# Kernel tuning notes

Hardware: AMD Instinct MI355X
Metric: run time of the kernel (lower is better)

Reference implementation:

```python
import jax, jax.numpy as jnp
import numpy as np
from jax.ops import segment_sum, segment_max

B, L, D, H, DK, NL, V, FF = 8, 256, 256, 8, 32, 4, 2048, 1024
N = B * L
EPS = 1e-5


def _ln(x, g, b):
    m = jnp.mean(x, -1, keepdims=True)
    v = jnp.var(x, -1, keepdims=True)
    return (x - m) * jax.lax.rsqrt(v + EPS) * g + b


def setup_inputs() -> dict:
    key = jax.random.key(0)
    ks = list(jax.random.split(key, 16))
    # causal decoder-decoder edges, sorted by destination (DGL 'dd' eids)
    dst_seq = np.repeat(np.arange(L), np.arange(L) + 1)
    src_seq = np.concatenate([np.arange(j + 1) for j in range(L)])
    src = jnp.asarray(np.concatenate([src_seq + b * L for b in range(B)]), jnp.int32)
    dst = jnp.asarray(np.concatenate([dst_seq + b * L for b in range(B)]), jnp.int32)
    tokens = jax.random.randint(ks[0], (N,), 0, V)
    positions = jnp.tile(jnp.arange(L), B)  # tgt[1]
    s = 0.02
    nrm = lambda k, sh: jax.random.normal(k, sh, jnp.float32) * s
    return {
        'tokens': tokens, 'positions': positions, 'src': src, 'dst': dst,
        'value_tab': nrm(ks[1], (V, D)),
        'coord_tab': nrm(ks[2], (3, D)),
        'pos_tab': nrm(ks[3], (L, D)),
        'ln1_g': jnp.ones((NL, D), jnp.float32), 'ln1_b': jnp.zeros((NL, D), jnp.float32),
        'Wq': nrm(ks[4], (NL, D, D)), 'Wk': nrm(ks[5], (NL, D, D)),
        'Wv': nrm(ks[6], (NL, D, D)), 'Wo': nrm(ks[7], (NL, D, D)),
        'ln2_g': jnp.ones((NL, D), jnp.float32), 'ln2_b': jnp.zeros((NL, D), jnp.float32),
        'W1': nrm(ks[8], (NL, D, FF)), 'b1': jnp.zeros((NL, FF), jnp.float32),
        'W2': nrm(ks[9], (NL, FF, D)), 'b2': jnp.zeros((NL, D), jnp.float32),
        'lnf_g': jnp.ones((D,), jnp.float32), 'lnf_b': jnp.zeros((D,), jnp.float32),
        'Wgen': nrm(ks[10], (D, V)), 'bgen': jnp.zeros((V,), jnp.float32),
    }


def reference(tokens, positions, src, dst, value_tab, coord_tab, pos_tab,
              ln1_g, ln1_b, Wq, Wk, Wv, Wo, ln2_g, ln2_b,
              W1, b1, W2, b2, lnf_g, lnf_b, Wgen, bgen):
    # embeddings: value*sqrt(d) + coord(pos%3) + pos(pos//3)
    x = value_tab[tokens] * jnp.sqrt(jnp.float32(D)) \
        + coord_tab[positions % 3] + pos_tab[positions // 3]
    inv_sqrt_dk = 1.0 / jnp.sqrt(jnp.float32(DK))
    for i in range(NL):
        # pre_func: layernorm + qkv projection, split heads
        xn = _ln(x, ln1_g[i], ln1_b[i])
        q = (xn @ Wq[i]).reshape(N, H, DK)
        k = (xn @ Wk[i]).reshape(N, H, DK)
        v = (xn @ Wv[i]).reshape(N, H, DK)
        # apply_edges(u_dot_v): per-edge, per-head score
        score = jnp.einsum('ehd,ehd->eh', k[src], q[dst]) * inv_sqrt_dk  # [E,H]
        # edge_softmax over edges grouped by destination node
        m = jax.lax.stop_gradient(
            segment_max(score, dst, num_segments=N, indices_are_sorted=True))
        a = jnp.exp(score - m[dst])
        denom = segment_sum(a, dst, num_segments=N, indices_are_sorted=True)
        alpha = a / denom[dst]  # [E,H]
        # send_and_recv(u_mul_e -> sum): softmax-weighted aggregation
        z = segment_sum(v[src] * alpha[..., None], dst,
                        num_segments=N, indices_are_sorted=True).reshape(N, D)
        # post_func: output proj + residual, then FFN sublayer
        x = x + z @ Wo[i]
        xn2 = _ln(x, ln2_g[i], ln2_b[i])
        x = x + (jax.nn.relu(xn2 @ W1[i] + b1[i]) @ W2[i] + b2[i])
    x = _ln(x, lnf_g, lnf_b)
    return jax.nn.log_softmax(x @ Wgen + bgen, axis=-1)  # generator
```

## Files before the change

kernel.cpp:

```cpp
#include <hip/hip_runtime.h>
#include <hip/hip_bf16.h>
#include <math.h>

constexpr int B_ = 8, L_ = 256, D_ = 256, H_ = 8, DK_ = 32, NL_ = 4, V_ = 2048, FF_ = 1024;
constexpr int N_ = B_ * L_;
constexpr float EPS_ = 1e-5f;
constexpr int LDW_ = 56;

typedef short bf16x8 __attribute__((ext_vector_type(8)));
typedef float f32x4 __attribute__((ext_vector_type(4)));
typedef _Float16 f16x4 __attribute__((ext_vector_type(4)));

__device__ __forceinline__ short f2b(float f) {
    union { __hip_bfloat16 h; short s; } u;
    u.h = __float2bfloat16(f);
    return u.s;
}

__global__ void transpose_all(const float* __restrict__ Wq, const float* __restrict__ Wk,
                              const float* __restrict__ Wv, const float* __restrict__ Wo,
                              const float* __restrict__ W1, const float* __restrict__ W2,
                              const float* __restrict__ Wgen,
                              short* __restrict__ wqT, short* __restrict__ wkT,
                              short* __restrict__ wvT, short* __restrict__ woT,
                              short* __restrict__ w1T, short* __restrict__ w2T,
                              short* __restrict__ wgT,
                              const int* __restrict__ tokens, const int* __restrict__ positions,
                              const float* __restrict__ vtab, const float* __restrict__ ctab,
                              const float* __restrict__ ptab, float* __restrict__ x) {
    __shared__ float tile[32][33];
    int id = blockIdx.x;
    if (id >= 3584) {
        int n = id - 3584;
        int d = threadIdx.y * 32 + threadIdx.x;
        int tok = tokens[n], p = positions[n];
        x[n * D_ + d] = vtab[tok * D_ + d] * 16.0f + ctab[(p % 3) * D_ + d] + ptab[(p / 3) * D_ + d];
        return;
    }
    const float* src;
    short* dst;
    int K, Nn, tx, ty;
    if (id < 1024) {
        int m = id >> 8, rem = id & 255, layer = rem >> 6, tt = rem & 63;
        K = 256; Nn = 256; tx = tt & 7; ty = tt >> 3;
        size_t off = (size_t)layer * 256 * 256;
        if (m == 0) { src = Wq + off; dst = wqT + off; }
        else if (m == 1) { src = Wk + off; dst = wkT + off; }
        else if (m == 2) { src = Wv + off; dst = wvT + off; }
        else { src = Wo + off; dst = woT + off; }
    } else if (id < 2048) {
        int rem = id - 1024, layer = rem >> 8, tt = rem & 255;
        K = 256; Nn = 1024; tx = tt & 31; ty = tt >> 5;
        size_t off = (size_t)layer * 256 * 1024;
        src = W1 + off; dst = w1T + off;
    } else if (id < 3072) {
        int rem = id - 2048, layer = rem >> 8, tt = rem & 255;
        K = 1024; Nn = 256; tx = tt & 7; ty = tt >> 3;
        size_t off = (size_t)layer * 1024 * 256;
        src = W2 + off; dst = w2T + off;
    } else {
        int tt = id - 3072;
        K = 256; Nn = 2048; tx = tt & 63; ty = tt >> 6;
        src = Wgen; dst = wgT;
    }
    int n0 = tx * 32, k0 = ty * 32;
    int x_ = threadIdx.x, y_ = threadIdx.y;
#pragma unroll
    for (int i = 0; i < 32; i += 8)
        tile[y_ + i][x_] = src[(size_t)(k0 + y_ + i) * Nn + n0 + x_];
    __syncthreads();
#pragma unroll
    for (int i = 0; i < 32; i += 8)
        dst[(size_t)(n0 + y_ + i) * K + k0 + x_] = f2b(tile[x_][y_ + i]);
}

__device__ __forceinline__ int4 pack8(const float* v) {
    union { short s[8]; int4 q; } u;
#pragma unroll
    for (int j = 0; j < 8; ++j) u.s[j] = f2b(v[j]);
    return u.q;
}

template <int EPI, bool HAS_BIAS>
__device__ __forceinline__ void gemm_epilogue(f32x4 acc00, f32x4 acc01, f32x4 acc10, f32x4 acc11,
                                              const float* __restrict__ bias, float* __restrict__ Cf,
                                              short* __restrict__ Cb, int Nout, int kz,
                                              int m0, int n0, int mo, int no, int quad, int r) {
#pragma unroll
    for (int i = 0; i < 2; ++i) {
#pragma unroll
        for (int j = 0; j < 2; ++j) {
            f32x4 acc = (i == 0) ? (j == 0 ? acc00 : acc01) : (j == 0 ? acc10 : acc11);
            int col = n0 + no + j * 16 + r;
            float bval = HAS_BIAS ? bias[col] : 0.f;
#pragma unroll
            for (int p = 0; p < 4; ++p) {
                int row = m0 + mo + i * 16 + quad * 4 + p;
                float v = acc[p];
                if (EPI == 1) {
                    Cb[(size_t)row * Nout + col] = f2b(fmaxf(v + bval, 0.f));
                } else if (EPI == 2) {
                    float add = v + ((HAS_BIAS && kz == 0) ? bval : 0.f);
                    atomicAdd(&Cf[(size_t)row * Nout + col], add);
                } else if (EPI == 3) {
                    Cf[(size_t)row * Nout + col] = v + bval;
                } else if (EPI == 4) {
                    Cb[(size_t)row * Nout + col] = f2b(v);
                } else {
                    ((_Float16*)Cb)[(size_t)row * Nout + col] = (_Float16)v;
                }
            }
        }
    }
}

template <int EPI, bool HAS_BIAS>
__device__ __forceinline__ void gemm_body(const short* __restrict__ A, const short* __restrict__ Bt,
                                          const float* __restrict__ bias, float* __restrict__ Cf,
                                          short* __restrict__ Cb, int M, int K, int Nout,
                                          int kbeg, int kend, int kz) {
    __shared__ short As[2][64][LDW_];
    __shared__ short Bs[2][64][LDW_];
    int t = threadIdx.x;
    int m0 = blockIdx.x * 64, n0 = blockIdx.y * 64;
    int sr = t >> 2, sc = (t & 3) * 8;
    int lane = t & 63, w = t >> 6;
    int mo = (w & 1) * 32, no = (w >> 1) * 32;
    int quad = lane >> 4, r = lane & 15;
    f32x4 acc00 = {}, acc01 = {}, acc10 = {}, acc11 = {};
    const short* Ap = &A[(size_t)(m0 + sr) * K + sc];
    const short* Bp = &Bt[(size_t)(n0 + sr) * K + sc];
    int4 av = *(const int4*)(Ap + kbeg);
    int4 bv = *(const int4*)(Bp + kbeg);
    *(int4*)&As[0][sr][sc] = av;
    *(int4*)&Bs[0][sr][sc] = bv;
    if (kbeg + 32 < kend) {
        av = *(const int4*)(Ap + kbeg + 32);
        bv = *(const int4*)(Bp + kbeg + 32);
    }
    __syncthreads();
    int p = 0;
    for (int k0 = kbeg; k0 < kend; k0 += 32, p ^= 1) {
        if (k0 + 32 < kend) {
            *(int4*)&As[p ^ 1][sr][sc] = av;
            *(int4*)&Bs[p ^ 1][sr][sc] = bv;
            if (k0 + 64 < kend) {
                av = *(const int4*)(Ap + k0 + 64);
                bv = *(const int4*)(Bp + k0 + 64);
            }
        }
        bf16x8 a0 = *(const bf16x8*)&As[p][mo + r][quad * 8];
        bf16x8 a1 = *(const bf16x8*)&As[p][mo + 16 + r][quad * 8];
        bf16x8 b0 = *(const bf16x8*)&Bs[p][no + r][quad * 8];
        bf16x8 b1 = *(const bf16x8*)&Bs[p][no + 16 + r][quad * 8];
        acc00 = __builtin_amdgcn_mfma_f32_16x16x32_bf16(a0, b0, acc00, 0, 0, 0);
        acc01 = __builtin_amdgcn_mfma_f32_16x16x32_bf16(a0, b1, acc01, 0, 0, 0);
        acc10 = __builtin_amdgcn_mfma_f32_16x16x32_bf16(a1, b0, acc10, 0, 0, 0);
        acc11 = __builtin_amdgcn_mfma_f32_16x16x32_bf16(a1, b1, acc11, 0, 0, 0);
        if (k0 + 32 < kend) __syncthreads();
    }
    gemm_epilogue<EPI, HAS_BIAS>(acc00, acc01, acc10, acc11, bias, Cf, Cb, Nout, kz,
                                 m0, n0, mo, no, quad, r);
}

template <int EPI, bool HAS_BIAS>
__device__ __forceinline__ void gemm_ln_body(const float* __restrict__ X,
                                             const float* __restrict__ lg, const float* __restrict__ lb,
                                             const short* __restrict__ Bt,
                                             const float* __restrict__ bias, float* __restrict__ Cf,
                                             short* __restrict__ Cb, int Nout) {
    __shared__ short As[2][64][LDW_];
    __shared__ short Bs[2][64][LDW_];
    __shared__ float gs[256], bs_[256];
    int t = threadIdx.x;
    int m0 = blockIdx.x * 64, n0 = blockIdx.y * 64;
    int sr = t >> 2, sc = (t & 3) * 8;
    int lane = t & 63, w = t >> 6;
    int mo = (w & 1) * 32, no = (w >> 1) * 32;
    int quad = lane >> 4, r = lane & 15;

    float xv[64];
    const float* xp = &X[(size_t)(m0 + sr) * 256 + sc];
#pragma unroll
    for (int c = 0; c < 8; ++c) {
        *(float4*)&xv[c * 8] = *(const float4*)(xp + c * 32);
        *(float4*)&xv[c * 8 + 4] = *(const float4*)(xp + c * 32 + 4);
    }
    const short* Bp = &Bt[(size_t)(n0 + sr) * 256 + sc];
    int4 bv = *(const int4*)Bp;
    gs[t] = lg[t];
    bs_[t] = lb[t];

    float s1 = 0.f, s2 = 0.f;
#pragma unroll
    for (int j = 0; j < 64; ++j) {
        s1 += xv[j];
        s2 += xv[j] * xv[j];
    }
    s1 += __shfl_xor(s1, 1, 64); s1 += __shfl_xor(s1, 2, 64);
    s2 += __shfl_xor(s2, 1, 64); s2 += __shfl_xor(s2, 2, 64);
    float mean = s1 * (1.0f / 256.0f);
    float inv = rsqrtf(s2 * (1.0f / 256.0f) - mean * mean + EPS_);
    __syncthreads();

    int4 a_regs[8];
#pragma unroll
    for (int c = 0; c < 8; ++c) {
        float tmp[8];
#pragma unroll
        for (int j = 0; j < 8; ++j)
            tmp[j] = (xv[c * 8 + j] - mean) * inv * gs[c * 32 + sc + j] + bs_[c * 32 + sc + j];
        a_regs[c] = pack8(tmp);
    }

    *(int4*)&As[0][sr][sc] = a_regs[0];
    *(int4*)&Bs[0][sr][sc] = bv;
    bv = *(const int4*)(Bp + 32);
    __syncthreads();

    f32x4 acc00 = {}, acc01 = {}, acc10 = {}, acc11 = {};
#pragma unroll
    for (int c = 0; c < 8; ++c) {
        int p = c & 1;
        if (c + 1 < 8) {
            *(int4*)&As[p ^ 1][sr][sc] = a_regs[c + 1];
            *(int4*)&Bs[p ^ 1][sr][sc] = bv;
            if (c + 2 < 8) bv = *(const int4*)(Bp + (c + 2) * 32);
        }
        bf16x8 a0 = *(const bf16x8*)&As[p][mo + r][quad * 8];
        bf16x8 a1 = *(const bf16x8*)&As[p][mo + 16 + r][quad * 8];
        bf16x8 b0 = *(const bf16x8*)&Bs[p][no + r][quad * 8];
        bf16x8 b1 = *(const bf16x8*)&Bs[p][no + 16 + r][quad * 8];
        acc00 = __builtin_amdgcn_mfma_f32_16x16x32_bf16(a0, b0, acc00, 0, 0, 0);
        acc01 = __builtin_amdgcn_mfma_f32_16x16x32_bf16(a0, b1, acc01, 0, 0, 0);
        acc10 = __builtin_amdgcn_mfma_f32_16x16x32_bf16(a1, b0, acc10, 0, 0, 0);
        acc11 = __builtin_amdgcn_mfma_f32_16x16x32_bf16(a1, b1, acc11, 0, 0, 0);
        if (c + 1 < 8) __syncthreads();
    }
    gemm_epilogue<EPI, HAS_BIAS>(acc00, acc01, acc10, acc11, bias, Cf, Cb, Nout, 0,
                                 m0, n0, mo, no, quad, r);
}

__global__ __launch_bounds__(256) void gemm_ln_qkv(const float* __restrict__ X,
                                                   const float* __restrict__ lg, const float* __restrict__ lb,
                                                   const short* __restrict__ wq, const short* __restrict__ wk,
                                                   const short* __restrict__ wv,
                                                   short* __restrict__ q, short* __restrict__ k,
                                                   short* __restrict__ v) {
    if (blockIdx.z == 0)
        gemm_ln_body<4, false>(X, lg, lb, wq, nullptr, nullptr, q, D_);
    else if (blockIdx.z == 1)
        gemm_ln_body<4, false>(X, lg, lb, wk, nullptr, nullptr, k, D_);
    else
        gemm_ln_body<5, false>(X, lg, lb, wv, nullptr, nullptr, v, D_);
}

__global__ __launch_bounds__(256) void gemm_ln_relu(const float* __restrict__ X,
                                                    const float* __restrict__ lg, const float* __restrict__ lb,
                                                    const short* __restrict__ Bt, const float* __restrict__ bias,
                                                    short* __restrict__ C) {
    gemm_ln_body<1, true>(X, lg, lb, Bt, bias, nullptr, C, FF_);
}

__global__ __launch_bounds__(256) void gemm_ln_bias(const float* __restrict__ X,
                                                    const float* __restrict__ lg, const float* __restrict__ lb,
                                                    const short* __restrict__ Bt, const float* __restrict__ bias,
                                                    float* __restrict__ C) {
    gemm_ln_body<3, true>(X, lg, lb, Bt, bias, C, nullptr, V_);
}

template <int SPLITK, bool HAS_BIAS>
__global__ __launch_bounds__(256) void gemm_accum(const short* __restrict__ A, const short* __restrict__ Bt,
                                                  const float* __restrict__ bias, float* __restrict__ C,
                                                  int M, int K, int Nout) {
    int Kp = K / SPLITK;
    int kz = blockIdx.z;
    gemm_body<2, HAS_BIAS>(A, Bt, bias, C, nullptr, M, K, Nout, kz * Kp, kz * Kp + Kp, kz);
}

__global__ __launch_bounds__(64) void attn_kernel(const short* __restrict__ q,
                                                  const short* __restrict__ k,
                                                  const _Float16* __restrict__ v,
                                                  short* __restrict__ z) {
    int blk = blockIdx.x;
    int bh = blk & 63;
    int qt = 15 - (blk >> 6);
    int b = bh >> 3, h = bh & 7;
    int lane = threadIdx.x;
    int r = lane & 15, quad = lane >> 4;
    int row0 = b * L_;

    bf16x8 qf = *(const bf16x8*)&q[(size_t)(row0 + qt * 16 + r) * D_ + h * DK_ + quad * 8];
    f32x4 O0 = {}, O1 = {};
    float mA = -1e30f, den = 0.f;
    int nk = qt + 1;

    bf16x8 kf = *(const bf16x8*)&k[(size_t)(row0 + r) * D_ + h * DK_ + quad * 8];
    f16x4 va, vb;
    {
        const _Float16* vp = v + (size_t)(row0 + quad * 4) * D_ + h * DK_;
#pragma unroll
        for (int i = 0; i < 4; ++i) {
            va[i] = vp[(size_t)i * D_ + r];
            vb[i] = vp[(size_t)i * D_ + 16 + r];
        }
    }
    for (int kt = 0; kt < nk; ++kt) {
        bf16x8 kf_n = kf;
        f16x4 va_n = va, vb_n = vb;
        if (kt + 1 < nk) {
            kf_n = *(const bf16x8*)&k[(size_t)(row0 + (kt + 1) * 16 + r) * D_ + h * DK_ + quad * 8];
            const _Float16* vp = v + (size_t)(row0 + (kt + 1) * 16 + quad * 4) * D_ + h * DK_;
#pragma unroll
            for (int i = 0; i < 4; ++i) {
                va_n[i] = vp[(size_t)i * D_ + r];
                vb_n[i] = vp[(size_t)i * D_ + 16 + r];
            }
        }
        f32x4 zero = {};
        f32x4 s = __builtin_amdgcn_mfma_f32_16x16x32_bf16(kf, qf, zero, 0, 0, 0);
#pragma unroll
        for (int i2 = 0; i2 < 4; ++i2) s[i2] *= 0.17677669529663687f;
        if (kt == qt) {
#pragma unroll
            for (int i2 = 0; i2 < 4; ++i2)
                if (quad * 4 + i2 > r) s[i2] = -1e30f;
        }
        float tmax = fmaxf(fmaxf(s[0], s[1]), fmaxf(s[2], s[3]));
        tmax = fmaxf(tmax, __shfl_xor(tmax, 16, 64));
        tmax = fmaxf(tmax, __shfl_xor(tmax, 32, 64));
        float mn = fmaxf(mA, tmax);
        float alpha = __expf(mA - mn);
        mA = mn;
        float p0 = __expf(s[0] - mn), p1 = __expf(s[1] - mn);
        float p2 = __expf(s[2] - mn), p3 = __expf(s[3] - mn);
        float ts = (p0 + p1) + (p2 + p3);
        ts += __shfl_xor(ts, 16, 64);
        ts += __shfl_xor(ts, 32, 64);
        den = den * alpha + ts;
        f16x4 pf;
        pf[0] = (_Float16)p0; pf[1] = (_Float16)p1; pf[2] = (_Float16)p2; pf[3] = (_Float16)p3;
        float al[4];
#pragma unroll
        for (int i2 = 0; i2 < 4; ++i2) al[i2] = __shfl(alpha, quad * 4 + i2, 64);
#pragma unroll
        for (int i2 = 0; i2 < 4; ++i2) { O0[i2] *= al[i2]; O1[i2] *= al[i2]; }
        O0 = __builtin_amdgcn_mfma_f32_16x16x16f16(pf, va, O0, 0, 0, 0);
        O1 = __builtin_amdgcn_mfma_f32_16x16x16f16(pf, vb, O1, 0, 0, 0);
        kf = kf_n; va = va_n; vb = vb_n;
    }
#pragma unroll
    for (int i2 = 0; i2 < 4; ++i2) {
        float inv = 1.0f / __shfl(den, quad * 4 + i2, 64);
        int rowz = row0 + qt * 16 + quad * 4 + i2;
        z[(size_t)rowz * D_ + h * DK_ + r] = f2b(O0[i2] * inv);
        z[(size_t)rowz * D_ + h * DK_ + 16 + r] = f2b(O1[i2] * inv);
    }
}

__global__ void lsm_kernel(float* __restrict__ logits) {
    __shared__ float rm[4], rs[4];
    int row = blockIdx.x, t = threadIdx.x;
    float* p = logits + (size_t)row * V_;
    float vals[8];
    float mx = -INFINITY;
#pragma unroll
    for (int i = 0; i < 8; ++i) {
        vals[i] = p[t + i * 256];
        mx = fmaxf(mx, vals[i]);
    }
#pragma unroll
    for (int off = 32; off; off >>= 1) mx = fmaxf(mx, __shfl_xor(mx, off, 64));
    int w = t >> 6;
    if ((t & 63) == 0) rm[w] = mx;
    __syncthreads();
    mx = fmaxf(fmaxf(rm[0], rm[1]), fmaxf(rm[2], rm[3]));
    float s = 0.f;
#pragma unroll
    for (int i = 0; i < 8; ++i) s += __expf(vals[i] - mx);
#pragma unroll
    for (int off = 32; off; off >>= 1) s += __shfl_xor(s, off, 64);
    if ((t & 63) == 0) rs[w] = s;
    __syncthreads();
    s = rs[0] + rs[1] + rs[2] + rs[3];
    float lse = mx + logf(s);
#pragma unroll
    for (int i = 0; i < 8; ++i) p[t + i * 256] = vals[i] - lse;
}

extern "C" void kernel_launch(void* const* d_in, const int* in_sizes, int n_in,
                              void* d_out, int out_size, void* d_ws, size_t ws_size,
                              hipStream_t stream) {
    const int* tokens = (const int*)d_in[0];
    const int* positions = (const int*)d_in[1];
    const float* vtab = (const float*)d_in[4];
    const float* ctab = (const float*)d_in[5];
    const float* ptab = (const float*)d_in[6];
    const float* ln1_g = (const float*)d_in[7];
    const float* ln1_b = (const float*)d_in[8];
    const float* Wq = (const float*)d_in[9];
    const float* Wk = (const float*)d_in[10];
    const float* Wv = (const float*)d_in[11];
    const float* Wo = (const float*)d_in[12];
    const float* ln2_g = (const float*)d_in[13];
    const float* ln2_b = (const float*)d_in[14];
    const float* W1 = (const float*)d_in[15];
    const float* b1 = (const float*)d_in[16];
    const float* W2 = (const float*)d_in[17];
    const float* b2 = (const float*)d_in[18];
    const float* lnf_g = (const float*)d_in[19];
    const float* lnf_b = (const float*)d_in[20];
    const float* Wgen = (const float*)d_in[21];
    const float* bgen = (const float*)d_in[22];

    char* p = (char*)d_ws;
    float* x = (float*)p;      p += (size_t)N_ * D_ * 4;
    short* qb = (short*)p;     p += (size_t)N_ * D_ * 4;
    short* kb = (short*)p;     p += (size_t)N_ * D_ * 4;
    short* vbh = (short*)p;    p += (size_t)N_ * D_ * 4;
    short* zbb = (short*)p;    p += (size_t)N_ * D_ * 2;
    short* hbb = (short*)p;    p += (size_t)N_ * FF_ * 2;
    short* wqT = (short*)p;    p += (size_t)NL_ * D_ * D_ * 2;
    short* wkT = (short*)p;    p += (size_t)NL_ * D_ * D_ * 2;
    short* wvT = (short*)p;    p += (size_t)NL_ * D_ * D_ * 2;
    short* woT = (short*)p;    p += (size_t)NL_ * D_ * D_ * 2;
    short* w1T = (short*)p;    p += (size_t)NL_ * D_ * FF_ * 2;
    short* w2T = (short*)p;    p += (size_t)NL_ * FF_ * D_ * 2;
    short* wgT = (short*)p;    p += (size_t)D_ * V_ * 2;
    float* out = (float*)d_out;

    dim3 tb(32, 8);
    transpose_all<<<5632, tb, 0, stream>>>(Wq, Wk, Wv, Wo, W1, W2, Wgen,
                                           wqT, wkT, wvT, woT, w1T, w2T, wgT,
                                           tokens, positions, vtab, ctab, ptab, x);

    dim3 gQKV(N_ / 64, D_ / 64, 3);
    dim3 gWo(N_ / 64, D_ / 64, 2);
    dim3 gW1(N_ / 64, FF_ / 64);
    dim3 gW2(N_ / 64, D_ / 64, 4);
    dim3 gGen(N_ / 64, V_ / 64);
    for (int i = 0; i < NL_; ++i) {
        gemm_ln_qkv<<<gQKV, 256, 0, stream>>>(x, ln1_g + i * D_, ln1_b + i * D_,
                                              wqT + (size_t)i * D_ * D_, wkT + (size_t)i * D_ * D_,
                                              wvT + (size_t)i * D_ * D_, qb, kb, vbh);
        attn_kernel<<<B_ * H_ * 16, 64, 0, stream>>>(qb, kb, (const _Float16*)vbh, zbb);
        gemm_accum<2, false><<<gWo, 256, 0, stream>>>(zbb, woT + (size_t)i * D_ * D_, nullptr, x, N_, D_, D_);
        gemm_ln_relu<<<gW1, 256, 0, stream>>>(x, ln2_g + i * D_, ln2_b + i * D_,
                                              w1T + (size_t)i * D_ * FF_, b1 + (size_t)i * FF_, hbb);
        gemm_accum<4, true><<<gW2, 256, 0, stream>>>(hbb, w2T + (size_t)i * FF_ * D_, b2 + (size_t)i * D_,
                                                     x, N_, FF_, D_);
    }
    gemm_ln_bias<<<gGen, 256, 0, stream>>>(x, lnf_g, lnf_b, wgT, bgen, out);
    lsm_kernel<<<N_, 256, 0, stream>>>(out);
}
```

Baseline: 306.1 us.

## Fuse LayerNorm, QKV projection and causal attention into one per-head kernel

Replaces the separate LN+QKV GEMM kernel and the attention kernel with one kernel that runs one 512-thread block per (batch, head). Each block normalizes its batch's rows and projects only that head's Q/K/V slice into LDS, then runs causal flash-style attention from LDS. Each wave handles two query tiles paired so the causal work is balanced. This removes a launch per layer and the global round trip for Q/K/V. In exchange the grid shrinks to 64 blocks, LayerNorm is recomputed once per head, and the kernel needs a large LDS footprint.

```diff
diff --git a/kernel.cpp b/kernel.cpp
--- a/kernel.cpp
+++ b/kernel.cpp
@@ -15,6 +15,13 @@
     union { __hip_bfloat16 h; short s; } u;
     u.h = __float2bfloat16(f);
     return u.s;
+}
+
+__device__ __forceinline__ int4 pack8(const float* v) {
+    union { short s[8]; int4 q; } u;
+#pragma unroll
+    for (int j = 0; j < 8; ++j) u.s[j] = f2b(v[j]);
+    return u.q;
 }
 
 __global__ void transpose_all(const float* __restrict__ Wq, const float* __restrict__ Wk,
@@ -74,13 +81,6 @@
         dst[(size_t)(n0 + y_ + i) * K + k0 + x_] = f2b(tile[x_][y_ + i]);
 }
 
-__device__ __forceinline__ int4 pack8(const float* v) {
-    union { short s[8]; int4 q; } u;
-#pragma unroll
-    for (int j = 0; j < 8; ++j) u.s[j] = f2b(v[j]);
-    return u.q;
-}
-
 template <int EPI, bool HAS_BIAS>
 __device__ __forceinline__ void gemm_epilogue(f32x4 acc00, f32x4 acc01, f32x4 acc10, f32x4 acc11,
                                               const float* __restrict__ bias, float* __restrict__ Cf,
@@ -241,20 +241,6 @@
                                  m0, n0, mo, no, quad, r);
 }
 
-__global__ __launch_bounds__(256) void gemm_ln_qkv(const float* __restrict__ X,
-                                                   const float* __restrict__ lg, const float* __restrict__ lb,
-                                                   const short* __restrict__ wq, const short* __restrict__ wk,
-                                                   const short* __restrict__ wv,
-                                                   short* __restrict__ q, short* __restrict__ k,
-                                                   short* __restrict__ v) {
-    if (blockIdx.z == 0)
-        gemm_ln_body<4, false>(X, lg, lb, wq, nullptr, nullptr, q, D_);
-    else if (blockIdx.z == 1)
-        gemm_ln_body<4, false>(X, lg, lb, wk, nullptr, nullptr, k, D_);
-    else
-        gemm_ln_body<5, false>(X, lg, lb, wv, nullptr, nullptr, v, D_);
-}
-
 __global__ __launch_bounds__(256) void gemm_ln_relu(const float* __restrict__ X,
                                                     const float* __restrict__ lg, const float* __restrict__ lb,
                                                     const short* __restrict__ Bt, const float* __restrict__ bias,
@@ -278,83 +264,142 @@
     gemm_body<2, HAS_BIAS>(A, Bt, bias, C, nullptr, M, K, Nout, kz * Kp, kz * Kp + Kp, kz);
 }
 
-__global__ __launch_bounds__(64) void attn_kernel(const short* __restrict__ q,
-                                                  const short* __restrict__ k,
-                                                  const _Float16* __restrict__ v,
-                                                  short* __restrict__ z) {
-    int blk = blockIdx.x;
-    int bh = blk & 63;
-    int qt = 15 - (blk >> 6);
+__global__ __launch_bounds__(512) void qkv_attn_kernel(const float* __restrict__ X,
+                                                       const float* __restrict__ lg,
+                                                       const float* __restrict__ lb,
+                                                       const short* __restrict__ wqT,
+                                                       const short* __restrict__ wkT,
+                                                       const short* __restrict__ wvT,
+                                                       short* __restrict__ z) {
+    __shared__ short Af[64][264];
+    __shared__ short Wsq[32][264], Wsk[32][264], Wsv[32][264];
+    __shared__ short qls[256][40], kls[256][40];
+    __shared__ _Float16 vls[256][40];
+    __shared__ float gsh[256], bsh[256];
+
+    int t = threadIdx.x;
+    int bh = blockIdx.x;
     int b = bh >> 3, h = bh & 7;
-    int lane = threadIdx.x;
-    int r = lane & 15, quad = lane >> 4;
     int row0 = b * L_;
-
-    bf16x8 qf = *(const bf16x8*)&q[(size_t)(row0 + qt * 16 + r) * D_ + h * DK_ + quad * 8];
-    f32x4 O0 = {}, O1 = {};
-    float mA = -1e30f, den = 0.f;
-    int nk = qt + 1;
-
-    bf16x8 kf = *(const bf16x8*)&k[(size_t)(row0 + r) * D_ + h * DK_ + quad * 8];
-    f16x4 va, vb;
+    int w = t >> 6, lane = t & 63;
+    int quad = lane >> 4, r = lane & 15;
+
+    if (t < 256) { gsh[t] = lg[t]; bsh[t] = lb[t]; }
     {
-        const _Float16* vp = v + (size_t)(row0 + quad * 4) * D_ + h * DK_;
+        int wr = t >> 4, wc = (t & 15) * 16;
+        const short* qs = &wqT[(size_t)(h * 32 + wr) * 256 + wc];
+        const short* ks = &wkT[(size_t)(h * 32 + wr) * 256 + wc];
+        const short* vs = &wvT[(size_t)(h * 32 + wr) * 256 + wc];
+        *(int4*)&Wsq[wr][wc] = *(const int4*)qs;
+        *(int4*)&Wsq[wr][wc + 8] = *(const int4*)(qs + 8);
+        *(int4*)&Wsk[wr][wc] = *(const int4*)ks;
+        *(int4*)&Wsk[wr][wc + 8] = *(const int4*)(ks + 8);
+        *(int4*)&Wsv[wr][wc] = *(const int4*)vs;
+        *(int4*)&Wsv[wr][wc + 8] = *(const int4*)(vs + 8);
+    }
+
+    int xrow = t >> 3, xcl = (t & 7) * 32;
+    int wm = (w & 3) * 16, wn = (w >> 2) * 16;
+    for (int c = 0; c < 4; ++c) {
+        float xv[32];
+        const float* xp = &X[(size_t)(row0 + c * 64 + xrow) * 256 + xcl];
+#pragma unroll
+        for (int i = 0; i < 8; ++i)
+            *(float4*)&xv[i * 4] = *(const float4*)(xp + i * 4);
+        float s1 = 0.f, s2 = 0.f;
+#pragma unroll
+        for (int j = 0; j < 32; ++j) {
+            s1 += xv[j];
+            s2 += xv[j] * xv[j];
+        }
+        s1 += __shfl_xor(s1, 1, 64); s1 += __shfl_xor(s1, 2, 64); s1 += __shfl_xor(s1, 4, 64);
+        s2 += __shfl_xor(s2, 1, 64); s2 += __shfl_xor(s2, 2, 64); s2 += __shfl_xor(s2, 4, 64);
+        float mean = s1 * (1.0f / 256.0f);
+        float inv = rsqrtf(s2 * (1.0f / 256.0f) - mean * mean + EPS_);
+        __syncthreads();
 #pragma unroll
         for (int i = 0; i < 4; ++i) {
-            va[i] = vp[(size_t)i * D_ + r];
-            vb[i] = vp[(size_t)i * D_ + 16 + r];
-        }
-    }
-    for (int kt = 0; kt < nk; ++kt) {
-        bf16x8 kf_n = kf;
-        f16x4 va_n = va, vb_n = vb;
-        if (kt + 1 < nk) {
-            kf_n = *(const bf16x8*)&k[(size_t)(row0 + (kt + 1) * 16 + r) * D_ + h * DK_ + quad * 8];
-            const _Float16* vp = v + (size_t)(row0 + (kt + 1) * 16 + quad * 4) * D_ + h * DK_;
+            float tmp[8];
+#pragma unroll
+            for (int j = 0; j < 8; ++j)
+                tmp[j] = (xv[i * 8 + j] - mean) * inv * gsh[xcl + i * 8 + j] + bsh[xcl + i * 8 + j];
+            *(int4*)&Af[xrow][xcl + i * 8] = pack8(tmp);
+        }
+        __syncthreads();
+        f32x4 aq = {}, ak = {}, av = {};
+#pragma unroll
+        for (int ks = 0; ks < 8; ++ks) {
+            bf16x8 a = *(const bf16x8*)&Af[wm + r][ks * 32 + quad * 8];
+            bf16x8 bq = *(const bf16x8*)&Wsq[wn + r][ks * 32 + quad * 8];
+            bf16x8 bk = *(const bf16x8*)&Wsk[wn + r][ks * 32 + quad * 8];
+            bf16x8 bv = *(const bf16x8*)&Wsv[wn + r][ks * 32 + quad * 8];
+            aq = __builtin_amdgcn_mfma_f32_16x16x32_bf16(a, bq, aq, 0, 0, 0);
+            ak = __builtin_amdgcn_mfma_f32_16x16x32_bf16(a, bk, ak, 0, 0, 0);
+            av = __builtin_amdgcn_mfma_f32_16x16x32_bf16(a, bv, av, 0, 0, 0);
+        }
+#pragma unroll
+        for (int p = 0; p < 4; ++p) {
+            int orow = c * 64 + wm + quad * 4 + p;
+            int ocol = wn + r;
+            qls[orow][ocol] = f2b(aq[p]);
+            kls[orow][ocol] = f2b(ak[p]);
+            vls[orow][ocol] = (_Float16)av[p];
+        }
+    }
+    __syncthreads();
+
+#pragma unroll
+    for (int tk = 0; tk < 2; ++tk) {
+        int qt = (tk == 0) ? w : 15 - w;
+        bf16x8 qf = *(const bf16x8*)&qls[qt * 16 + r][quad * 8];
+        f32x4 O0 = {}, O1 = {};
+        float mA = -1e30f, den = 0.f;
+        for (int kt = 0; kt <= qt; ++kt) {
+            bf16x8 kf = *(const bf16x8*)&kls[kt * 16 + r][quad * 8];
+            f16x4 va, vb;
 #pragma unroll
             for (int i = 0; i < 4; ++i) {
-                va_n[i] = vp[(size_t)i * D_ + r];
-                vb_n[i] = vp[(size_t)i * D_ + 16 + r];
+                va[i] = vls[kt * 16 + quad * 4 + i][r];
+                vb[i] = vls[kt * 16 + quad * 4 + i][16 + r];
             }
-        }
-        f32x4 zero = {};
-        f32x4 s = __builtin_amdgcn_mfma_f32_16x16x32_bf16(kf, qf, zero, 0, 0, 0);
-#pragma unroll
-        for (int i2 = 0; i2 < 4; ++i2) s[i2] *= 0.17677669529663687f;
-        if (kt == qt) {
-#pragma unroll
-            for (int i2 = 0; i2 < 4; ++i2)
-                if (quad * 4 + i2 > r) s[i2] = -1e30f;
-        }
-        float tmax = fmaxf(fmaxf(s[0], s[1]), fmaxf(s[2], s[3]));
-        tmax = fmaxf(tmax, __shfl_xor(tmax, 16, 64));
-        tmax = fmaxf(tmax, __shfl_xor(tmax, 32, 64));
-        float mn = fmaxf(mA, tmax);
-        float alpha = __expf(mA - mn);
-        mA = mn;
-        float p0 = __expf(s[0] - mn), p1 = __expf(s[1] - mn);
-        float p2 = __expf(s[2] - mn), p3 = __expf(s[3] - mn);
-        float ts = (p0 + p1) + (p2 + p3);
-        ts += __shfl_xor(ts, 16, 64);
-        ts += __shfl_xor(ts, 32, 64);
-        den = den * alpha + ts;
-        f16x4 pf;
-        pf[0] = (_Float16)p0; pf[1] = (_Float16)p1; pf[2] = (_Float16)p2; pf[3] = (_Float16)p3;
-        float al[4];
-#pragma unroll
-        for (int i2 = 0; i2 < 4; ++i2) al[i2] = __shfl(alpha, quad * 4 + i2, 64);
-#pragma unroll
-        for (int i2 = 0; i2 < 4; ++i2) { O0[i2] *= al[i2]; O1[i2] *= al[i2]; }
-        O0 = __builtin_amdgcn_mfma_f32_16x16x16f16(pf, va, O0, 0, 0, 0);
-        O1 = __builtin_amdgcn_mfma_f32_16x16x16f16(pf, vb, O1, 0, 0, 0);
-        kf = kf_n; va = va_n; vb = vb_n;
-    }
-#pragma unroll
-    for (int i2 = 0; i2 < 4; ++i2) {
-        float inv = 1.0f / __shfl(den, quad * 4 + i2, 64);
-        int rowz = row0 + qt * 16 + quad * 4 + i2;
-        z[(size_t)rowz * D_ + h * DK_ + r] = f2b(O0[i2] * inv);
-        z[(size_t)rowz * D_ + h * DK_ + 16 + r] = f2b(O1[i2] * inv);
+            f32x4 zero = {};
+            f32x4 s = __builtin_amdgcn_mfma_f32_16x16x32_bf16(kf, qf, zero, 0, 0, 0);
+#pragma unroll
+            for (int i2 = 0; i2 < 4; ++i2) s[i2] *= 0.17677669529663687f;
+            if (kt == qt) {
+#pragma unroll
+                for (int i2 = 0; i2 < 4; ++i2)
+                    if (quad * 4 + i2 > r) s[i2] = -1e30f;
+            }
+            float tmax = fmaxf(fmaxf(s[0], s[1]), fmaxf(s[2], s[3]));
+            tmax = fmaxf(tmax, __shfl_xor(tmax, 16, 64));
+            tmax = fmaxf(tmax, __shfl_xor(tmax, 32, 64));
+            float mn = fmaxf(mA, tmax);
+            float alpha = __expf(mA - mn);
+            mA = mn;
+            float p0 = __expf(s[0] - mn), p1 = __expf(s[1] - mn);
+            float p2 = __expf(s[2] - mn), p3 = __expf(s[3] - mn);
+            float ts = (p0 + p1) + (p2 + p3);
+            ts += __shfl_xor(ts, 16, 64);
+            ts += __shfl_xor(ts, 32, 64);
+            den = den * alpha + ts;
+            f16x4 pf;
+            pf[0] = (_Float16)p0; pf[1] = (_Float16)p1; pf[2] = (_Float16)p2; pf[3] = (_Float16)p3;
+            float al[4];
+#pragma unroll
+            for (int i2 = 0; i2 < 4; ++i2) al[i2] = __shfl(alpha, quad * 4 + i2, 64);
+#pragma unroll
+            for (int i2 = 0; i2 < 4; ++i2) { O0[i2] *= al[i2]; O1[i2] *= al[i2]; }
+            O0 = __builtin_amdgcn_mfma_f32_16x16x16f16(pf, va, O0, 0, 0, 0);
+            O1 = __builtin_amdgcn_mfma_f32_16x16x16f16(pf, vb, O1, 0, 0, 0);
+        }
+#pragma unroll
+        for (int i2 = 0; i2 < 4; ++i2) {
+            float inv = 1.0f / __shfl(den, quad * 4 + i2, 64);
+            int rowz = row0 + qt * 16 + quad * 4 + i2;
+            z[(size_t)rowz * D_ + h * DK_ + r] = f2b(O0[i2] * inv);
+            z[(size_t)rowz * D_ + h * DK_ + 16 + r] = f2b(O1[i2] * inv);
+        }
     }
 }
 
@@ -415,9 +460,6 @@
 
     char* p = (char*)d_ws;
     float* x = (float*)p;      p += (size_t)N_ * D_ * 4;
-    short* qb = (short*)p;     p += (size_t)N_ * D_ * 4;
-    short* kb = (short*)p;     p += (size_t)N_ * D_ * 4;
-    short* vbh = (short*)p;    p += (size_t)N_ * D_ * 4;
     short* zbb = (short*)p;    p += (size_t)N_ * D_ * 2;
     short* hbb = (short*)p;    p += (size_t)N_ * FF_ * 2;
     short* wqT = (short*)p;    p += (size_t)NL_ * D_ * D_ * 2;
@@ -434,16 +476,15 @@
                                            wqT, wkT, wvT, woT, w1T, w2T, wgT,
                                            tokens, positions, vtab, ctab, ptab, x);
 
-    dim3 gQKV(N_ / 64, D_ / 64, 3);
     dim3 gWo(N_ / 64, D_ / 64, 2);
     dim3 gW1(N_ / 64, FF_ / 64);
     dim3 gW2(N_ / 64, D_ / 64, 4);
     dim3 gGen(N_ / 64, V_ / 64);
     for (int i = 0; i < NL_; ++i) {
-        gemm_ln_qkv<<<gQKV, 256, 0, stream>>>(x, ln1_g + i * D_, ln1_b + i * D_,
-                                              wqT + (size_t)i * D_ * D_, wkT + (size_t)i * D_ * D_,
-                                              wvT + (size_t)i * D_ * D_, qb, kb, vbh);
-        attn_kernel<<<B_ * H_ * 16, 64, 0, stream>>>(qb, kb, (const _Float16*)vbh, zbb);
+        qkv_attn_kernel<<<B_ * H_, 512, 0, stream>>>(x, ln1_g + i * D_, ln1_b + i * D_,
+                                                     wqT + (size_t)i * D_ * D_,
+                                                     wkT + (size_t)i * D_ * D_,
+                                                     wvT + (size_t)i * D_ * D_, zbb);
         gemm_accum<2, false><<<gWo, 256, 0, stream>>>(zbb, woT + (size_t)i * D_ * D_, nullptr, x, N_, D_, D_);
         gemm_ln_relu<<<gW1, 256, 0, stream>>>(x, ln2_g + i * D_, ln2_b + i * D_,
                                               w1T + (size_t)i * D_ * FF_, b1 + (size_t)i * FF_, hbb);
```

Measured after the change: 326.2 us. 6.6% more time.
